# Kernel optimization log

Hardware: AMD Instinct MI355X
Metric: run time of the kernel (lower is better)

## Reference

```python
import jax, jax.numpy as jnp
import numpy as np

B, NNODES = 65536, 32
D_IN, D_G, D_C, H, D_OUT = 16, 8, 16, 64, 4


def setup_inputs() -> dict:
    key = jax.random.key(0)
    ks = jax.random.split(key, 24)
    N = B * NNODES
    x = jax.random.normal(ks[0], (N, D_IN), jnp.float32)
    other_obs = jax.random.normal(ks[1], (B, D_C), jnp.float32)
    # star graph per batch element with reverse edges: (0->j) and (j->0)
    bs = np.concatenate([np.zeros(NNODES - 1, np.int32), np.arange(1, NNODES, dtype=np.int32)])
    bd = np.concatenate([np.arange(1, NNODES, dtype=np.int32), np.zeros(NNODES - 1, np.int32)])
    offs = (np.arange(B, dtype=np.int32) * NNODES)[:, None]
    src = jnp.asarray((bs[None, :] + offs).reshape(-1))
    dst = jnp.asarray((bd[None, :] + offs).reshape(-1))
    node_seg = jnp.asarray(np.repeat(np.arange(B, dtype=np.int32), NNODES))
    s = 0.1
    p = lambda k, sh: jax.random.normal(k, sh, jnp.float32) * s
    return dict(
        x=x, other_obs=other_obs, src=src, dst=dst, node_seg=node_seg,
        Wp1=p(ks[2], (D_IN, D_G)), bp1=jnp.zeros((D_G,), jnp.float32),
        Ws1=p(ks[3], (D_IN, D_G)), Wn1=p(ks[4], (D_G, D_G)), bc1=jnp.zeros((D_G,), jnp.float32),
        Wp2=p(ks[5], (D_G, D_G)), bp2=jnp.zeros((D_G,), jnp.float32),
        Ws2=p(ks[6], (D_G, D_G)), Wn2=p(ks[7], (D_G, D_G)), bc2=jnp.zeros((D_G,), jnp.float32),
        W1=p(ks[8], (D_C + D_G, H)), bf1=jnp.zeros((H,), jnp.float32),
        W2=p(ks[9], (H, H)), bf2=jnp.zeros((H,), jnp.float32),
        W3=p(ks[10], (H, H)), bf3=jnp.zeros((H,), jnp.float32),
        W4=jax.random.uniform(ks[11], (H, D_OUT), jnp.float32, -0.003, 0.003),
        bf4=jnp.zeros((D_OUT,), jnp.float32),
    )


def _sage_pool(h, src, dst, Wp, bp, Ws, Wn, bc, num_nodes):
    # DGL SAGEConv aggregator_type='pool': relu(fc_pool(h_src)), scatter-max to dst
    m = jax.nn.relu(h @ Wp + bp)[src]              # [E, D_G]
    agg = jax.ops.segment_max(m, dst, num_segments=num_nodes)
    agg = jnp.where(jnp.isfinite(agg), agg, 0.0)   # empty-neighbor nodes -> 0 (DGL default)
    return h @ Ws + agg @ Wn + bc


def reference(x, other_obs, src, dst, node_seg,
              Wp1, bp1, Ws1, Wn1, bc1,
              Wp2, bp2, Ws2, Wn2, bc2,
              W1, bf1, W2, bf2, W3, bf3, W4, bf4):
    N = x.shape[0]
    Bn = other_obs.shape[0]
    n_per = N // Bn
    h = jnp.tanh(_sage_pool(x, src, dst, Wp1, bp1, Ws1, Wn1, bc1, N))  # conv1 activation=tanh
    h = _sage_pool(h, src, dst, Wp2, bp2, Ws2, Wn2, bc2, N)            # conv2, no activation
    pooled = jax.ops.segment_sum(h, node_seg, num_segments=Bn) / n_per  # AvgPooling (fixed n)
    res = jnp.concatenate([pooled, other_obs], axis=1)
    h1 = jax.nn.relu(res @ W1 + bf1)
    h2 = jax.nn.relu(h1 @ W2 + bf2)
    h3 = jax.nn.relu(h2 @ W3 + bf3)
    return jnp.tanh(h3 @ W4 + bf4)
```

## Files before the change

### kernel.cpp

```cpp
#include <hip/hip_runtime.h>

#define OFF_CW1   0
#define OFF_BP1   256
#define OFF_BC1   264
#define OFF_WN1   272
#define OFF_CW2   336
#define OFF_BP2   400
#define OFF_A     408
#define OFF_C     920
#define OFF_W1B   1432
#define OFF_BF1P  2456
#define OFF_W2    2520
#define OFF_BF2   6616
#define OFF_W3    6680
#define OFF_BF3   10776
#define OFF_W4    10840
#define OFF_BF4   11096
#define RES_OFF   16384

__device__ __forceinline__ float fast_tanh(float v) {
  v = fminf(fmaxf(v, -10.f), 10.f);
  float e = exp2f(v * 2.8853900817779268f);
  return 1.f - 2.f * __builtin_amdgcn_rcpf(e + 1.f);
}

template<int PAT>
__device__ __forceinline__ float swzf(float v) {
  return __int_as_float(__builtin_amdgcn_ds_swizzle(__float_as_int(v), PAT));
}
__device__ __forceinline__ float bfly_max32(float t) {
  t = fmaxf(t, swzf<0x041F>(t));
  t = fmaxf(t, swzf<0x081F>(t));
  t = fmaxf(t, swzf<0x101F>(t));
  t = fmaxf(t, swzf<0x201F>(t));
  t = fmaxf(t, swzf<0x401F>(t));
  return t;
}
__device__ __forceinline__ float bfly_sum32(float t) {
  t += swzf<0x041F>(t);
  t += swzf<0x081F>(t);
  t += swzf<0x101F>(t);
  t += swzf<0x201F>(t);
  t += swzf<0x401F>(t);
  return t;
}
__device__ __forceinline__ float bcast0_32(float t) { return swzf<0x0000>(t); }

__global__ void setup_blob(const float* __restrict__ Wp1, const float* __restrict__ bp1,
                           const float* __restrict__ Ws1, const float* __restrict__ Wn1,
                           const float* __restrict__ bc1,
                           const float* __restrict__ Wp2, const float* __restrict__ bp2,
                           const float* __restrict__ Ws2, const float* __restrict__ Wn2,
                           const float* __restrict__ bc2,
                           const float* __restrict__ W1, const float* __restrict__ bf1,
                           const float* __restrict__ W2, const float* __restrict__ bf2,
                           const float* __restrict__ W3, const float* __restrict__ bf3,
                           const float* __restrict__ W4, const float* __restrict__ bf4,
                           float* __restrict__ blob) {
  const int t = threadIdx.x;
  if (t < 128) { int f = t >> 3, g = t & 7;
    blob[OFF_CW1 + f*16 + g]     = Wp1[f*8 + g];
    blob[OFF_CW1 + f*16 + 8 + g] = Ws1[f*8 + g];
  }
  if (t < 8) { blob[OFF_BP1+t] = bp1[t]; blob[OFF_BC1+t] = bc1[t]; blob[OFF_BP2+t] = bp2[t]; }
  if (t < 64) { blob[OFF_WN1+t] = Wn1[t]; blob[OFF_CW2+t] = Wp2[t]; }
  if (t < 4)  { blob[OFF_BF4+t] = bf4[t]; }
  blob[OFF_W4 + t] = W4[t];
  for (int idx = t; idx < 4096; idx += 256) {
    blob[OFF_W2 + idx] = W2[idx];
    blob[OFF_W3 + idx] = W3[idx];
  }
  for (int idx = t; idx < 1024; idx += 256) blob[OFF_W1B + idx] = W1[512 + idx];
  if (t < 64) {
    const int o = t;
    float accB = bf1[o];
    for (int k = 0; k < 8; k++) accB += bc2[k] * W1[k*64 + o];
    blob[OFF_BF1P + o] = accB;
    for (int j = 0; j < 8; j++) {
      float a = 0.f, c = 0.f;
      for (int k = 0; k < 8; k++) {
        a += Ws2[j*8 + k] * W1[k*64 + o];
        c += Wn2[j*8 + k] * W1[k*64 + o];
      }
      blob[OFF_A + j*64 + o] = a * (1.f/32.f);
      blob[OFF_C + j*64 + o] = c * (1.f/32.f);
    }
    blob[OFF_BF2 + o] = bf2[o];
    blob[OFF_BF3 + o] = bf3[o];
  }
}

__global__ __launch_bounds__(256, 4) void conv_kernel(const float* __restrict__ x,
                                                      const float* __restrict__ wb,
                                                      float* __restrict__ res) {
  const int lane = threadIdx.x & 63;
  const int pair = blockIdx.x * 4 + (threadIdx.x >> 6);
  const int s = lane >> 5, n = lane & 31;
  const int b = pair * 2 + s;

  const float4* xp = (const float4*)(x + ((size_t)b * 32 + n) * 16);
  float4 a0 = xp[0], a1 = xp[1], a2 = xp[2], a3 = xp[3];
  float xr[16] = {a0.x,a0.y,a0.z,a0.w, a1.x,a1.y,a1.z,a1.w,
                  a2.x,a2.y,a2.z,a2.w, a3.x,a3.y,a3.z,a3.w};
  float m[8], sp[8];
  #pragma unroll
  for (int g = 0; g < 8; g++) { m[g] = wb[OFF_BP1+g]; sp[g] = wb[OFF_BC1+g]; }
  #pragma unroll
  for (int f = 0; f < 16; f++) {
    #pragma unroll
    for (int g = 0; g < 8; g++) {
      m[g]  = fmaf(xr[f], wb[OFF_CW1 + f*16 + g],     m[g]);
      sp[g] = fmaf(xr[f], wb[OFF_CW1 + f*16 + 8 + g], sp[g]);
    }
  }
  #pragma unroll
  for (int g = 0; g < 8; g++) m[g] = fmaxf(m[g], 0.f);

  float agg[8];
  #pragma unroll
  for (int g = 0; g < 8; g++) {
    float t = (n == 0) ? 0.f : m[g];
    t = bfly_max32(t);
    float m0 = bcast0_32(m[g]);
    agg[g] = (n == 0) ? t : m0;
  }
  #pragma unroll
  for (int j = 0; j < 8; j++)
    #pragma unroll
    for (int g = 0; g < 8; g++)
      sp[g] = fmaf(agg[j], wb[OFF_WN1 + j*8 + g], sp[g]);

  float h[8];
  #pragma unroll
  for (int g = 0; g < 8; g++) h[g] = fast_tanh(sp[g]);

  float m2[8];
  #pragma unroll
  for (int g = 0; g < 8; g++) m2[g] = wb[OFF_BP2+g];
  #pragma unroll
  for (int j = 0; j < 8; j++)
    #pragma unroll
    for (int g = 0; g < 8; g++)
      m2[g] = fmaf(h[j], wb[OFF_CW2 + j*8 + g], m2[g]);
  #pragma unroll
  for (int g = 0; g < 8; g++) m2[g] = fmaxf(m2[g], 0.f);

  float outv[16];
  #pragma unroll
  for (int g = 0; g < 8; g++) {
    float t = (n == 0) ? 0.f : m2[g];
    t = bfly_max32(t);
    float m20 = bcast0_32(m2[g]);
    outv[8+g] = t + 31.f * m20;
    outv[g] = bfly_sum32(h[g]);
  }
  if (n == 0) {
    float4* rp = (float4*)(res + (size_t)b * 16);
    rp[0] = make_float4(outv[0], outv[1], outv[2], outv[3]);
    rp[1] = make_float4(outv[4], outv[5], outv[6], outv[7]);
    rp[2] = make_float4(outv[8], outv[9], outv[10], outv[11]);
    rp[3] = make_float4(outv[12], outv[13], outv[14], outv[15]);
  }
}

#define HSTR 65
__global__ __launch_bounds__(256, 3) void mlp_kernel(const float* __restrict__ res,
                                                     const float* __restrict__ obs,
                                                     const float* __restrict__ wb,
                                                     float* __restrict__ out) {
  __shared__ float hx[64 * HSTR];
  const int lane = threadIdx.x & 63;
  const int p    = __builtin_amdgcn_readfirstlane(threadIdx.x >> 6);
  const int b    = blockIdx.x * 64 + lane;
  const int ob0  = p * 16;

  const float4* rp = (const float4*)(res + (size_t)b * 16);
  float4 r0 = rp[0], r1 = rp[1], r2 = rp[2], r3 = rp[3];
  const float4* op = (const float4*)(obs + (size_t)b * 16);
  float4 o0 = op[0], o1 = op[1], o2 = op[2], o3 = op[3];
  float rm[8] = {r0.x,r0.y,r0.z,r0.w, r1.x,r1.y,r1.z,r1.w};
  float ag[8] = {r2.x,r2.y,r2.z,r2.w, r3.x,r3.y,r3.z,r3.w};
  float ob[16] = {o0.x,o0.y,o0.z,o0.w, o1.x,o1.y,o1.z,o1.w,
                  o2.x,o2.y,o2.z,o2.w, o3.x,o3.y,o3.z,o3.w};

  float acc[16];
  #pragma unroll
  for (int i = 0; i < 16; i++) acc[i] = wb[OFF_BF1P + ob0 + i];
  #pragma unroll
  for (int j = 0; j < 8; j++)
    #pragma unroll
    for (int i = 0; i < 16; i++) acc[i] = fmaf(rm[j], wb[OFF_A + j*64 + ob0 + i], acc[i]);
  #pragma unroll
  for (int j = 0; j < 8; j++)
    #pragma unroll
    for (int i = 0; i < 16; i++) acc[i] = fmaf(ag[j], wb[OFF_C + j*64 + ob0 + i], acc[i]);
  #pragma unroll
  for (int j = 0; j < 16; j++)
    #pragma unroll
    for (int i = 0; i < 16; i++) acc[i] = fmaf(ob[j], wb[OFF_W1B + j*64 + ob0 + i], acc[i]);
  #pragma unroll
  for (int i = 0; i < 16; i++) hx[lane*HSTR + ob0 + i] = fmaxf(acc[i], 0.f);
  __syncthreads();
  float h[64];
  #pragma unroll
  for (int k = 0; k < 64; k++) h[k] = hx[lane*HSTR + k];
  __syncthreads();

  #pragma unroll
  for (int i = 0; i < 16; i++) acc[i] = wb[OFF_BF2 + ob0 + i];
  #pragma unroll
  for (int k = 0; k < 64; k++)
    #pragma unroll
    for (int i = 0; i < 16; i++) acc[i] = fmaf(h[k], wb[OFF_W2 + k*64 + ob0 + i], acc[i]);
  #pragma unroll
  for (int i = 0; i < 16; i++) hx[lane*HSTR + ob0 + i] = fmaxf(acc[i], 0.f);
  __syncthreads();
  #pragma unroll
  for (int k = 0; k < 64; k++) h[k] = hx[lane*HSTR + k];
  __syncthreads();

  #pragma unroll
  for (int i = 0; i < 16; i++) acc[i] = wb[OFF_BF3 + ob0 + i];
  #pragma unroll
  for (int k = 0; k < 64; k++)
    #pragma unroll
    for (int i = 0; i < 16; i++) acc[i] = fmaf(h[k], wb[OFF_W3 + k*64 + ob0 + i], acc[i]);
  #pragma unroll
  for (int i = 0; i < 16; i++) hx[lane*HSTR + ob0 + i] = fmaxf(acc[i], 0.f);
  __syncthreads();

  if (p == 0) {
    #pragma unroll
    for (int k = 0; k < 64; k++) h[k] = hx[lane*HSTR + k];
    float o4[4];
    #pragma unroll
    for (int d = 0; d < 4; d++) o4[d] = wb[OFF_BF4 + d];
    #pragma unroll
    for (int k = 0; k < 64; k++)
      #pragma unroll
      for (int d = 0; d < 4; d++) o4[d] = fmaf(h[k], wb[OFF_W4 + k*4 + d], o4[d]);
    #pragma unroll
    for (int d = 0; d < 4; d++) o4[d] = fast_tanh(o4[d]);
    ((float4*)out)[b] = make_float4(o4[0], o4[1], o4[2], o4[3]);
  }
}

extern "C" void kernel_launch(void* const* d_in, const int* in_sizes, int n_in,
                              void* d_out, int out_size, void* d_ws, size_t ws_size,
                              hipStream_t stream) {
  const float* x   = (const float*)d_in[0];
  const float* obs = (const float*)d_in[1];
  const float* Wp1 = (const float*)d_in[5];
  const float* bp1 = (const float*)d_in[6];
  const float* Ws1 = (const float*)d_in[7];
  const float* Wn1 = (const float*)d_in[8];
  const float* bc1 = (const float*)d_in[9];
  const float* Wp2 = (const float*)d_in[10];
  const float* bp2 = (const float*)d_in[11];
  const float* Ws2 = (const float*)d_in[12];
  const float* Wn2 = (const float*)d_in[13];
  const float* bc2 = (const float*)d_in[14];
  const float* W1  = (const float*)d_in[15];
  const float* bf1 = (const float*)d_in[16];
  const float* W2  = (const float*)d_in[17];
  const float* bf2 = (const float*)d_in[18];
  const float* W3  = (const float*)d_in[19];
  const float* bf3 = (const float*)d_in[20];
  const float* W4  = (const float*)d_in[21];
  const float* bf4 = (const float*)d_in[22];

  float* blob = (float*)d_ws;
  float* res  = (float*)d_ws + RES_OFF;
  float* out  = (float*)d_out;

  hipLaunchKernelGGL(setup_blob, dim3(1), dim3(256), 0, stream,
                     Wp1, bp1, Ws1, Wn1, bc1, Wp2, bp2, Ws2, Wn2, bc2,
                     W1, bf1, W2, bf2, W3, bf3, W4, bf4, blob);
  hipLaunchKernelGGL(conv_kernel, dim3(8192), dim3(256), 0, stream, x, blob, res);
  hipLaunchKernelGGL(mlp_kernel, dim3(1024), dim3(256), 0, stream, res, obs, blob, out);
}
```

Measured before the change: 283.1 us.

## Fuse setup, conv and MLP kernels into one kernel with LDS handoff

Replaces the three launches (weight blob setup, conv, MLP) with a single kernel. Each block processes 64 graphs: every wave loops over 8 pairs of graphs with software-prefetched x loads, writes per-graph summaries to LDS, then runs the MLP from LDS. The weight folding is recomputed per thread instead of precomputed, and weights are read directly from the inputs. This removes the intermediate global round-trip and two launch overheads, at the cost of fewer blocks (1024) with serialized conv work per wave and lower occupancy (launch bounds 2), which may expose HBM latency on the dominant x stream.

```diff
diff --git a/kernel.cpp b/kernel.cpp
--- a/kernel.cpp
+++ b/kernel.cpp
@@ -1,22 +1,5 @@
 #include <hip/hip_runtime.h>
 
-#define OFF_CW1   0
-#define OFF_BP1   256
-#define OFF_BC1   264
-#define OFF_WN1   272
-#define OFF_CW2   336
-#define OFF_BP2   400
-#define OFF_A     408
-#define OFF_C     920
-#define OFF_W1B   1432
-#define OFF_BF1P  2456
-#define OFF_W2    2520
-#define OFF_BF2   6616
-#define OFF_W3    6680
-#define OFF_BF3   10776
-#define OFF_W4    10840
-#define OFF_BF4   11096
-#define RES_OFF   16384
 
 __device__ __forceinline__ float fast_tanh(float v) {
   v = fminf(fmaxf(v, -10.f), 10.f);
@@ -46,202 +29,183 @@
 }
 __device__ __forceinline__ float bcast0_32(float t) { return swzf<0x0000>(t); }
 
-__global__ void setup_blob(const float* __restrict__ Wp1, const float* __restrict__ bp1,
-                           const float* __restrict__ Ws1, const float* __restrict__ Wn1,
-                           const float* __restrict__ bc1,
-                           const float* __restrict__ Wp2, const float* __restrict__ bp2,
-                           const float* __restrict__ Ws2, const float* __restrict__ Wn2,
-                           const float* __restrict__ bc2,
-                           const float* __restrict__ W1, const float* __restrict__ bf1,
-                           const float* __restrict__ W2, const float* __restrict__ bf2,
-                           const float* __restrict__ W3, const float* __restrict__ bf3,
-                           const float* __restrict__ W4, const float* __restrict__ bf4,
-                           float* __restrict__ blob) {
-  const int t = threadIdx.x;
-  if (t < 128) { int f = t >> 3, g = t & 7;
-    blob[OFF_CW1 + f*16 + g]     = Wp1[f*8 + g];
-    blob[OFF_CW1 + f*16 + 8 + g] = Ws1[f*8 + g];
+#define RSTR 17
+#define HSTR 65
+
+__global__ __launch_bounds__(256, 2) void fused_gnn(
+    const float* __restrict__ x,   const float* __restrict__ obs,
+    const float* __restrict__ Wp1, const float* __restrict__ bp1,
+    const float* __restrict__ Ws1, const float* __restrict__ Wn1,
+    const float* __restrict__ bc1,
+    const float* __restrict__ Wp2, const float* __restrict__ bp2,
+    const float* __restrict__ Ws2, const float* __restrict__ Wn2,
+    const float* __restrict__ bc2,
+    const float* __restrict__ W1,  const float* __restrict__ bf1,
+    const float* __restrict__ W2,  const float* __restrict__ bf2,
+    const float* __restrict__ W3,  const float* __restrict__ bf3,
+    const float* __restrict__ W4,  const float* __restrict__ bf4,
+    float* __restrict__ out) {
+  __shared__ float resT[64 * RSTR];
+  __shared__ float hx[64 * HSTR];
+
+  const int tid  = threadIdx.x;
+  const int lane = tid & 63;
+  const int p    = __builtin_amdgcn_readfirstlane(tid >> 6);
+  const int s    = lane >> 5, n = lane & 31;
+  const int b0   = blockIdx.x * 64;
+
+  const float4* op = (const float4*)(obs + (size_t)(b0 + lane) * 16);
+  float4 o0 = op[0], o1 = op[1], o2 = op[2], o3 = op[3];
+
+  const float* xb = x + (((size_t)(b0 + p * 16 + s)) * 32 + n) * 16;
+  float4 c0, c1, c2, c3;
+  { const float4* xp = (const float4*)xb; c0 = xp[0]; c1 = xp[1]; c2 = xp[2]; c3 = xp[3]; }
+
+  for (int j = 0; j < 8; ++j) {
+    float4 nx0, nx1, nx2, nx3;
+    if (j < 7) {
+      const float4* xp = (const float4*)(xb + (size_t)(j + 1) * 1024);
+      nx0 = xp[0]; nx1 = xp[1]; nx2 = xp[2]; nx3 = xp[3];
+    }
+    float xr[16] = {c0.x,c0.y,c0.z,c0.w, c1.x,c1.y,c1.z,c1.w,
+                    c2.x,c2.y,c2.z,c2.w, c3.x,c3.y,c3.z,c3.w};
+
+    float m[8], sp[8];
+    #pragma unroll
+    for (int g = 0; g < 8; g++) { m[g] = bp1[g]; sp[g] = bc1[g]; }
+    #pragma unroll
+    for (int f = 0; f < 16; f++) {
+      #pragma unroll
+      for (int g = 0; g < 8; g++) {
+        m[g]  = fmaf(xr[f], Wp1[f * 8 + g], m[g]);
+        sp[g] = fmaf(xr[f], Ws1[f * 8 + g], sp[g]);
+      }
+    }
+    #pragma unroll
+    for (int g = 0; g < 8; g++) m[g] = fmaxf(m[g], 0.f);
+
+    float agg[8];
+    #pragma unroll
+    for (int g = 0; g < 8; g++) {
+      float t = (n == 0) ? 0.f : m[g];
+      t = bfly_max32(t);
+      float m0 = bcast0_32(m[g]);
+      agg[g] = (n == 0) ? t : m0;
+    }
+    #pragma unroll
+    for (int jj = 0; jj < 8; jj++)
+      #pragma unroll
+      for (int g = 0; g < 8; g++)
+        sp[g] = fmaf(agg[jj], Wn1[jj * 8 + g], sp[g]);
+
+    float h[8];
+    #pragma unroll
+    for (int g = 0; g < 8; g++) h[g] = fast_tanh(sp[g]);
+
+    float m2[8];
+    #pragma unroll
+    for (int g = 0; g < 8; g++) m2[g] = bp2[g];
+    #pragma unroll
+    for (int jj = 0; jj < 8; jj++)
+      #pragma unroll
+      for (int g = 0; g < 8; g++)
+        m2[g] = fmaf(h[jj], Wp2[jj * 8 + g], m2[g]);
+    #pragma unroll
+    for (int g = 0; g < 8; g++) m2[g] = fmaxf(m2[g], 0.f);
+
+    float outv[16];
+    #pragma unroll
+    for (int g = 0; g < 8; g++) {
+      float t = (n == 0) ? 0.f : m2[g];
+      t = bfly_max32(t);
+      float m20 = bcast0_32(m2[g]);
+      outv[8 + g] = t + 31.f * m20;
+      outv[g] = bfly_sum32(h[g]);
+    }
+    if (n == 0) {
+      const int bib = (p * 8 + j) * 2 + s;
+      #pragma unroll
+      for (int i = 0; i < 16; i++) resT[bib * RSTR + i] = outv[i];
+    }
+    if (j < 7) { c0 = nx0; c1 = nx1; c2 = nx2; c3 = nx3; }
   }
-  if (t < 8) { blob[OFF_BP1+t] = bp1[t]; blob[OFF_BC1+t] = bc1[t]; blob[OFF_BP2+t] = bp2[t]; }
-  if (t < 64) { blob[OFF_WN1+t] = Wn1[t]; blob[OFF_CW2+t] = Wp2[t]; }
-  if (t < 4)  { blob[OFF_BF4+t] = bf4[t]; }
-  blob[OFF_W4 + t] = W4[t];
-  for (int idx = t; idx < 4096; idx += 256) {
-    blob[OFF_W2 + idx] = W2[idx];
-    blob[OFF_W3 + idx] = W3[idx];
-  }
-  for (int idx = t; idx < 1024; idx += 256) blob[OFF_W1B + idx] = W1[512 + idx];
-  if (t < 64) {
-    const int o = t;
-    float accB = bf1[o];
-    for (int k = 0; k < 8; k++) accB += bc2[k] * W1[k*64 + o];
-    blob[OFF_BF1P + o] = accB;
-    for (int j = 0; j < 8; j++) {
-      float a = 0.f, c = 0.f;
-      for (int k = 0; k < 8; k++) {
-        a += Ws2[j*8 + k] * W1[k*64 + o];
-        c += Wn2[j*8 + k] * W1[k*64 + o];
-      }
-      blob[OFF_A + j*64 + o] = a * (1.f/32.f);
-      blob[OFF_C + j*64 + o] = c * (1.f/32.f);
-    }
-    blob[OFF_BF2 + o] = bf2[o];
-    blob[OFF_BF3 + o] = bf3[o];
-  }
-}
-
-__global__ __launch_bounds__(256, 4) void conv_kernel(const float* __restrict__ x,
-                                                      const float* __restrict__ wb,
-                                                      float* __restrict__ res) {
-  const int lane = threadIdx.x & 63;
-  const int pair = blockIdx.x * 4 + (threadIdx.x >> 6);
-  const int s = lane >> 5, n = lane & 31;
-  const int b = pair * 2 + s;
-
-  const float4* xp = (const float4*)(x + ((size_t)b * 32 + n) * 16);
-  float4 a0 = xp[0], a1 = xp[1], a2 = xp[2], a3 = xp[3];
-  float xr[16] = {a0.x,a0.y,a0.z,a0.w, a1.x,a1.y,a1.z,a1.w,
-                  a2.x,a2.y,a2.z,a2.w, a3.x,a3.y,a3.z,a3.w};
-  float m[8], sp[8];
-  #pragma unroll
-  for (int g = 0; g < 8; g++) { m[g] = wb[OFF_BP1+g]; sp[g] = wb[OFF_BC1+g]; }
-  #pragma unroll
-  for (int f = 0; f < 16; f++) {
-    #pragma unroll
-    for (int g = 0; g < 8; g++) {
-      m[g]  = fmaf(xr[f], wb[OFF_CW1 + f*16 + g],     m[g]);
-      sp[g] = fmaf(xr[f], wb[OFF_CW1 + f*16 + 8 + g], sp[g]);
-    }
-  }
-  #pragma unroll
-  for (int g = 0; g < 8; g++) m[g] = fmaxf(m[g], 0.f);
-
-  float agg[8];
-  #pragma unroll
-  for (int g = 0; g < 8; g++) {
-    float t = (n == 0) ? 0.f : m[g];
-    t = bfly_max32(t);
-    float m0 = bcast0_32(m[g]);
-    agg[g] = (n == 0) ? t : m0;
-  }
-  #pragma unroll
-  for (int j = 0; j < 8; j++)
-    #pragma unroll
-    for (int g = 0; g < 8; g++)
-      sp[g] = fmaf(agg[j], wb[OFF_WN1 + j*8 + g], sp[g]);
-
-  float h[8];
-  #pragma unroll
-  for (int g = 0; g < 8; g++) h[g] = fast_tanh(sp[g]);
-
-  float m2[8];
-  #pragma unroll
-  for (int g = 0; g < 8; g++) m2[g] = wb[OFF_BP2+g];
-  #pragma unroll
-  for (int j = 0; j < 8; j++)
-    #pragma unroll
-    for (int g = 0; g < 8; g++)
-      m2[g] = fmaf(h[j], wb[OFF_CW2 + j*8 + g], m2[g]);
-  #pragma unroll
-  for (int g = 0; g < 8; g++) m2[g] = fmaxf(m2[g], 0.f);
-
-  float outv[16];
-  #pragma unroll
-  for (int g = 0; g < 8; g++) {
-    float t = (n == 0) ? 0.f : m2[g];
-    t = bfly_max32(t);
-    float m20 = bcast0_32(m2[g]);
-    outv[8+g] = t + 31.f * m20;
-    outv[g] = bfly_sum32(h[g]);
-  }
-  if (n == 0) {
-    float4* rp = (float4*)(res + (size_t)b * 16);
-    rp[0] = make_float4(outv[0], outv[1], outv[2], outv[3]);
-    rp[1] = make_float4(outv[4], outv[5], outv[6], outv[7]);
-    rp[2] = make_float4(outv[8], outv[9], outv[10], outv[11]);
-    rp[3] = make_float4(outv[12], outv[13], outv[14], outv[15]);
-  }
-}
-
-#define HSTR 65
-__global__ __launch_bounds__(256, 3) void mlp_kernel(const float* __restrict__ res,
-                                                     const float* __restrict__ obs,
-                                                     const float* __restrict__ wb,
-                                                     float* __restrict__ out) {
-  __shared__ float hx[64 * HSTR];
-  const int lane = threadIdx.x & 63;
-  const int p    = __builtin_amdgcn_readfirstlane(threadIdx.x >> 6);
-  const int b    = blockIdx.x * 64 + lane;
-  const int ob0  = p * 16;
-
-  const float4* rp = (const float4*)(res + (size_t)b * 16);
-  float4 r0 = rp[0], r1 = rp[1], r2 = rp[2], r3 = rp[3];
-  const float4* op = (const float4*)(obs + (size_t)b * 16);
-  float4 o0 = op[0], o1 = op[1], o2 = op[2], o3 = op[3];
-  float rm[8] = {r0.x,r0.y,r0.z,r0.w, r1.x,r1.y,r1.z,r1.w};
-  float ag[8] = {r2.x,r2.y,r2.z,r2.w, r3.x,r3.y,r3.z,r3.w};
+  __syncthreads();
+
+  const int ob0 = p * 16;
+  float rm[8], ag[8];
+  #pragma unroll
+  for (int jj = 0; jj < 8; jj++) { rm[jj] = resT[lane * RSTR + jj]; ag[jj] = resT[lane * RSTR + 8 + jj]; }
   float ob[16] = {o0.x,o0.y,o0.z,o0.w, o1.x,o1.y,o1.z,o1.w,
                   o2.x,o2.y,o2.z,o2.w, o3.x,o3.y,o3.z,o3.w};
 
+  float pooled[8];
+  #pragma unroll
+  for (int g = 0; g < 8; g++) pooled[g] = bc2[g] * 32.f;
+  #pragma unroll
+  for (int jj = 0; jj < 8; jj++)
+    #pragma unroll
+    for (int g = 0; g < 8; g++) {
+      pooled[g] = fmaf(rm[jj], Ws2[jj * 8 + g], pooled[g]);
+      pooled[g] = fmaf(ag[jj], Wn2[jj * 8 + g], pooled[g]);
+    }
+  #pragma unroll
+  for (int g = 0; g < 8; g++) pooled[g] *= (1.f / 32.f);
+
   float acc[16];
   #pragma unroll
-  for (int i = 0; i < 16; i++) acc[i] = wb[OFF_BF1P + ob0 + i];
-  #pragma unroll
-  for (int j = 0; j < 8; j++)
-    #pragma unroll
-    for (int i = 0; i < 16; i++) acc[i] = fmaf(rm[j], wb[OFF_A + j*64 + ob0 + i], acc[i]);
-  #pragma unroll
-  for (int j = 0; j < 8; j++)
-    #pragma unroll
-    for (int i = 0; i < 16; i++) acc[i] = fmaf(ag[j], wb[OFF_C + j*64 + ob0 + i], acc[i]);
-  #pragma unroll
-  for (int j = 0; j < 16; j++)
-    #pragma unroll
-    for (int i = 0; i < 16; i++) acc[i] = fmaf(ob[j], wb[OFF_W1B + j*64 + ob0 + i], acc[i]);
-  #pragma unroll
-  for (int i = 0; i < 16; i++) hx[lane*HSTR + ob0 + i] = fmaxf(acc[i], 0.f);
+  for (int i = 0; i < 16; i++) acc[i] = bf1[ob0 + i];
+  #pragma unroll
+  for (int jj = 0; jj < 8; jj++)
+    #pragma unroll
+    for (int i = 0; i < 16; i++) acc[i] = fmaf(pooled[jj], W1[jj * 64 + ob0 + i], acc[i]);
+  #pragma unroll
+  for (int jj = 0; jj < 16; jj++)
+    #pragma unroll
+    for (int i = 0; i < 16; i++) acc[i] = fmaf(ob[jj], W1[(8 + jj) * 64 + ob0 + i], acc[i]);
+  #pragma unroll
+  for (int i = 0; i < 16; i++) hx[lane * HSTR + ob0 + i] = fmaxf(acc[i], 0.f);
   __syncthreads();
   float h[64];
   #pragma unroll
-  for (int k = 0; k < 64; k++) h[k] = hx[lane*HSTR + k];
-  __syncthreads();
-
-  #pragma unroll
-  for (int i = 0; i < 16; i++) acc[i] = wb[OFF_BF2 + ob0 + i];
+  for (int k = 0; k < 64; k++) h[k] = hx[lane * HSTR + k];
+  __syncthreads();
+
+  #pragma unroll
+  for (int i = 0; i < 16; i++) acc[i] = bf2[ob0 + i];
   #pragma unroll
   for (int k = 0; k < 64; k++)
     #pragma unroll
-    for (int i = 0; i < 16; i++) acc[i] = fmaf(h[k], wb[OFF_W2 + k*64 + ob0 + i], acc[i]);
-  #pragma unroll
-  for (int i = 0; i < 16; i++) hx[lane*HSTR + ob0 + i] = fmaxf(acc[i], 0.f);
-  __syncthreads();
-  #pragma unroll
-  for (int k = 0; k < 64; k++) h[k] = hx[lane*HSTR + k];
-  __syncthreads();
-
-  #pragma unroll
-  for (int i = 0; i < 16; i++) acc[i] = wb[OFF_BF3 + ob0 + i];
+    for (int i = 0; i < 16; i++) acc[i] = fmaf(h[k], W2[k * 64 + ob0 + i], acc[i]);
+  #pragma unroll
+  for (int i = 0; i < 16; i++) hx[lane * HSTR + ob0 + i] = fmaxf(acc[i], 0.f);
+  __syncthreads();
+  #pragma unroll
+  for (int k = 0; k < 64; k++) h[k] = hx[lane * HSTR + k];
+  __syncthreads();
+
+  #pragma unroll
+  for (int i = 0; i < 16; i++) acc[i] = bf3[ob0 + i];
   #pragma unroll
   for (int k = 0; k < 64; k++)
     #pragma unroll
-    for (int i = 0; i < 16; i++) acc[i] = fmaf(h[k], wb[OFF_W3 + k*64 + ob0 + i], acc[i]);
-  #pragma unroll
-  for (int i = 0; i < 16; i++) hx[lane*HSTR + ob0 + i] = fmaxf(acc[i], 0.f);
+    for (int i = 0; i < 16; i++) acc[i] = fmaf(h[k], W3[k * 64 + ob0 + i], acc[i]);
+  #pragma unroll
+  for (int i = 0; i < 16; i++) hx[lane * HSTR + ob0 + i] = fmaxf(acc[i], 0.f);
   __syncthreads();
 
   if (p == 0) {
     #pragma unroll
-    for (int k = 0; k < 64; k++) h[k] = hx[lane*HSTR + k];
+    for (int k = 0; k < 64; k++) h[k] = hx[lane * HSTR + k];
     float o4[4];
     #pragma unroll
-    for (int d = 0; d < 4; d++) o4[d] = wb[OFF_BF4 + d];
+    for (int d = 0; d < 4; d++) o4[d] = bf4[d];
     #pragma unroll
     for (int k = 0; k < 64; k++)
       #pragma unroll
-      for (int d = 0; d < 4; d++) o4[d] = fmaf(h[k], wb[OFF_W4 + k*4 + d], o4[d]);
+      for (int d = 0; d < 4; d++) o4[d] = fmaf(h[k], W4[k * 4 + d], o4[d]);
     #pragma unroll
     for (int d = 0; d < 4; d++) o4[d] = fast_tanh(o4[d]);
-    ((float4*)out)[b] = make_float4(o4[0], o4[1], o4[2], o4[3]);
+    ((float4*)out)[b0 + lane] = make_float4(o4[0], o4[1], o4[2], o4[3]);
   }
 }
 
@@ -268,14 +232,9 @@
   const float* bf3 = (const float*)d_in[20];
   const float* W4  = (const float*)d_in[21];
   const float* bf4 = (const float*)d_in[22];
-
-  float* blob = (float*)d_ws;
-  float* res  = (float*)d_ws + RES_OFF;
-  float* out  = (float*)d_out;
-
-  hipLaunchKernelGGL(setup_blob, dim3(1), dim3(256), 0, stream,
-                     Wp1, bp1, Ws1, Wn1, bc1, Wp2, bp2, Ws2, Wn2, bc2,
-                     W1, bf1, W2, bf2, W3, bf3, W4, bf4, blob);
-  hipLaunchKernelGGL(conv_kernel, dim3(8192), dim3(256), 0, stream, x, blob, res);
-  hipLaunchKernelGGL(mlp_kernel, dim3(1024), dim3(256), 0, stream, res, obs, blob, out);
-}
+  float* out = (float*)d_out;
+
+  hipLaunchKernelGGL(fused_gnn, dim3(1024), dim3(256), 0, stream,
+                     x, obs, Wp1, bp1, Ws1, Wn1, bc1, Wp2, bp2, Ws2, Wn2, bc2,
+                     W1, bf1, W2, bf2, W3, bf3, W4, bf4, out);
+}
```

Result: slower. 369.7 us (+30.6%).
